# Optimization experiments

Measured on AMD Instinct MI355X. Metric: run time of the kernel, lower is better.

## Reference

```python
import jax, jax.numpy as jnp
import numpy as np

HIDDEN = 450
DEPTH = 4
ATOM_FDIM = 35
BOND_FDIM = 5
MAX_NB = 15
N_ATOMS = 30000
N_BONDS = 60000
N_MESS = 10001
N_MOLS = 1000
EPS = 1e-5


def setup_inputs() -> dict:
    key = jax.random.key(0)
    ks = jax.random.split(key, 10)
    fatoms = jax.random.normal(ks[0], (N_ATOMS, ATOM_FDIM), dtype=jnp.float32)
    fbonds = jax.random.normal(ks[1], (N_BONDS, ATOM_FDIM + BOND_FDIM), dtype=jnp.float32)
    # indices into concatenated [tree_message; graph_message] table (index 0 = zero pad slot)
    agraph = jax.random.randint(ks[2], (N_ATOMS, MAX_NB), 0, N_MESS + N_BONDS)
    bgraph = jax.random.randint(ks[3], (N_BONDS, MAX_NB), 0, N_MESS + N_BONDS)
    per_mol = N_ATOMS // N_MOLS
    starts = jnp.arange(N_MOLS, dtype=jnp.int64) * per_mol
    lens = jnp.full((N_MOLS,), per_mol, dtype=jnp.int64)
    scope = jnp.stack([starts, lens], axis=1)
    tree_message = jax.random.normal(ks[4], (N_MESS, HIDDEN), dtype=jnp.float32)
    tree_message = tree_message.at[0].set(0.0)  # padding row
    s = 0.05
    W_i = jax.random.normal(ks[5], (HIDDEN, ATOM_FDIM + BOND_FDIM), dtype=jnp.float32) * s
    W_h = jax.random.normal(ks[6], (HIDDEN, HIDDEN), dtype=jnp.float32) * s
    W_o = jax.random.normal(ks[7], (HIDDEN, ATOM_FDIM + HIDDEN), dtype=jnp.float32) * s
    b_o = jax.random.normal(ks[8], (HIDDEN,), dtype=jnp.float32) * s
    gamma = jnp.ones((HIDDEN,), dtype=jnp.float32)
    beta = jnp.zeros((HIDDEN,), dtype=jnp.float32)
    return {"fatoms": fatoms, "fbonds": fbonds, "agraph": agraph, "bgraph": bgraph,
            "scope": scope, "tree_message": tree_message, "W_i": W_i, "W_h": W_h,
            "W_o": W_o, "b_o": b_o, "gamma": gamma, "beta": beta}


def reference(fatoms, fbonds, agraph, bgraph, scope, tree_message, W_i, W_h, W_o, b_o, gamma, beta):
    # bond input features -> hidden
    binput = fbonds @ W_i.T                      # [n_bonds, H]
    graph_message = jax.nn.relu(binput)
    # message-passing loop (dropout is identity in eval / p=0)
    for _ in range(DEPTH - 1):
        message = jnp.concatenate([tree_message, graph_message], axis=0)
        nei = message[bgraph].sum(axis=1)        # padded-neighbor gather + sum -> [n_bonds, H]
        graph_message = jax.nn.relu(binput + nei @ W_h.T)
    message = jnp.concatenate([tree_message, graph_message], axis=0)
    nei = message[agraph].sum(axis=1)            # [n_atoms, H]
    ainput = jnp.concatenate([fatoms, nei], axis=1)
    h = ainput @ W_o.T + b_o                     # [n_atoms, H]
    # BatchNorm1d (training-mode batch statistics, biased variance)
    mean = h.mean(axis=0)
    var = ((h - mean) ** 2).mean(axis=0)
    h = (h - mean) * jax.lax.rsqrt(var + EPS) * gamma + beta
    h = jax.nn.relu(h)
    # scope-based segment mean pooling
    starts = scope[:, 0]
    lens = scope[:, 1]
    mol_id = jnp.searchsorted(starts, jnp.arange(N_ATOMS), side="right") - 1
    sums = jax.ops.segment_sum(h, mol_id, num_segments=N_MOLS)
    denom = jnp.maximum(lens, 1).astype(h.dtype)[:, None]
    return jnp.where(lens[:, None] > 0, sums / denom, jnp.zeros_like(sums))
```

## Files before the change

### kernel.cpp

```cpp
#include <hip/hip_runtime.h>
#include <cstdint>
#include <cstddef>

#define HIDDEN 450
#define ATOM_FDIM 35
#define IN_FDIM 40
#define MAX_NB 15
#define N_ATOMS 30000
#define N_BONDS 60000
#define N_MESS 10001
#define N_MOLS 1000
#define DEPTH 4
#define NTOT (N_MESS + N_BONDS)

#define KPAD 512
#define MLD  464
#define MB_PAD 60032
#define MA_PAD 30080

typedef _Float16 f16x8_t __attribute__((ext_vector_type(8)));
typedef float f32x4_t __attribute__((ext_vector_type(4)));
typedef unsigned short ushort8_t __attribute__((ext_vector_type(8)));

__device__ __forceinline__ float h2f(unsigned short u) {
    return (float)__builtin_bit_cast(_Float16, u);
}
__device__ __forceinline__ unsigned short f2h(float f) {
    return __builtin_bit_cast(unsigned short, (_Float16)f);
}
__device__ __forceinline__ void st_out(unsigned short* p, float v) { *p = f2h(v); }
__device__ __forceinline__ void st_out(float* p, float v) { *p = v; }

__device__ __forceinline__ void g2l16(const unsigned short* g, unsigned short* l) {
    __builtin_amdgcn_global_load_lds(
        (const __attribute__((address_space(1))) void*)g,
        (__attribute__((address_space(3))) void*)l, 16, 0, 0);
}

__device__ __forceinline__ bool sniff_is64(const void* g) {
    const int* g32 = (const int*)g;
    return (g32[1] | g32[3] | g32[5] | g32[7]) == 0;
}
__device__ __forceinline__ long long load_idx(const void* g, size_t pos, bool is64) {
    return is64 ? ((const long long*)g)[pos] : (long long)((const int*)g)[pos];
}

__global__ void zero_stats_kernel(float* __restrict__ p) {
    int i = blockIdx.x * blockDim.x + threadIdx.x;
    if (i < 2 * HIDDEN) p[i] = 0.f;
}

__global__ void build_wih_kernel(const float* __restrict__ W_i,
                                 const float* __restrict__ W_h,
                                 unsigned short* __restrict__ Wih) {
    int t = blockIdx.x * blockDim.x + threadIdx.x;
    if (t >= KPAD * KPAD) return;
    int n = t >> 9, k = t & 511;
    float v = 0.f;
    if (n < HIDDEN) {
        if (k < IN_FDIM)            v = W_i[(size_t)n * IN_FDIM + k];
        else if (k < IN_FDIM + HIDDEN) v = W_h[(size_t)n * HIDDEN + (k - IN_FDIM)];
    }
    Wih[t] = f2h(v);
}

__global__ void build_wo_kernel(const float* __restrict__ W_o,
                                unsigned short* __restrict__ Wo) {
    int t = blockIdx.x * blockDim.x + threadIdx.x;
    if (t >= KPAD * KPAD) return;
    int n = t >> 9, k = t & 511;
    float v = 0.f;
    if (n < HIDDEN) {
        if (k < ATOM_FDIM)                   v = W_o[(size_t)n * (ATOM_FDIM + HIDDEN) + k];
        else if (k >= IN_FDIM && k < IN_FDIM + HIDDEN)
            v = W_o[(size_t)n * (ATOM_FDIM + HIDDEN) + ATOM_FDIM + (k - IN_FDIM)];
    }
    Wo[t] = f2h(v);
}

__global__ void cvt_fbonds_kernel(const float* __restrict__ fbonds,
                                  unsigned short* __restrict__ Ab) {
    int t = blockIdx.x * blockDim.x + threadIdx.x;
    if (t >= MB_PAD * 64) return;
    int r = t >> 6, c8 = (t & 63) * 8;
    ushort8_t o;
    #pragma unroll
    for (int j = 0; j < 8; ++j) {
        int c = c8 + j;
        float v = (r < N_BONDS && c < IN_FDIM) ? fbonds[(size_t)r * IN_FDIM + c] : 0.f;
        o[j] = f2h(v);
    }
    *(ushort8_t*)(Ab + (size_t)r * KPAD + c8) = o;
}

__global__ void cvt_fatoms_kernel(const float* __restrict__ fatoms,
                                  unsigned short* __restrict__ Aa) {
    int t = blockIdx.x * blockDim.x + threadIdx.x;
    if (t >= MA_PAD * 64) return;
    int r = t >> 6, c8 = (t & 63) * 8;
    ushort8_t o;
    #pragma unroll
    for (int j = 0; j < 8; ++j) {
        int c = c8 + j;
        float v = (r < N_ATOMS && c < ATOM_FDIM) ? fatoms[(size_t)r * ATOM_FDIM + c] : 0.f;
        o[j] = f2h(v);
    }
    *(ushort8_t*)(Aa + (size_t)r * KPAD + c8) = o;
}

__global__ void cvt_tree_kernel(const float* __restrict__ tree,
                                unsigned short* __restrict__ tb) {
    int t = blockIdx.x * blockDim.x + threadIdx.x;
    if (t >= N_MESS * (MLD / 8)) return;
    int r = t / (MLD / 8), c8 = (t % (MLD / 8)) * 8;
    ushort8_t o;
    #pragma unroll
    for (int j = 0; j < 8; ++j) {
        int c = c8 + j;
        float v = (c < HIDDEN) ? tree[(size_t)r * HIDDEN + c] : 0.f;
        o[j] = f2h(v);
    }
    *(ushort8_t*)(tb + (size_t)r * MLD + c8) = o;
}

__global__ void zero_gmpad_kernel(unsigned short* __restrict__ gm) {
    int r = blockIdx.x * blockDim.x + threadIdx.x;
    if (r >= N_BONDS) return;
    ushort8_t z = {0, 0, 0, 0, 0, 0, 0, 0};
    *(ushort8_t*)(gm + (size_t)r * MLD + 448) = z;
    *(ushort8_t*)(gm + (size_t)r * MLD + 456) = z;
}

template<bool RELU, bool BIAS, typename OT>
__global__ __launch_bounds__(256)
void mfma_gemm_kernel(const unsigned short* __restrict__ A,
                      const unsigned short* __restrict__ B,
                      const float* __restrict__ bias,
                      OT* __restrict__ Out, int ldo,
                      int M, int Nvalid, int K)
{
    __shared__ unsigned short As[128 * 32];
    __shared__ unsigned short Bs[128 * 32];
    const int tid  = threadIdx.x;
    const int wave = tid >> 6, lane = tid & 63;
    const int m0 = blockIdx.x * 128, n0 = blockIdx.y * 128;
    const int wm = wave >> 1, wn = wave & 1;

    const unsigned short* At = A + (size_t)m0 * KPAD;
    const unsigned short* Bt = B + (size_t)n0 * KPAD;

    const int c0 = wave * 128 + lane;
    const int c1 = c0 + 64;
    const int rA0 = c0 >> 2, kc0 = (c0 & 3) * 8;
    const int rA1 = c1 >> 2, kc1 = (c1 & 3) * 8;
    unsigned short* lA0 = &As[(size_t)(wave * 128) * 8];
    unsigned short* lA1 = &As[(size_t)(wave * 128 + 64) * 8];
    unsigned short* lB0 = &Bs[(size_t)(wave * 128) * 8];
    unsigned short* lB1 = &Bs[(size_t)(wave * 128 + 64) * 8];

    const int fr = lane & 15, kof = (lane >> 4) * 8;

    f32x4_t acc[4][4];
    #pragma unroll
    for (int mi = 0; mi < 4; ++mi)
        #pragma unroll
        for (int ni = 0; ni < 4; ++ni)
            acc[mi][ni] = f32x4_t{0.f, 0.f, 0.f, 0.f};

    for (int k0 = 0; k0 < K; k0 += 32) {
        g2l16(At + (size_t)rA0 * KPAD + k0 + kc0, lA0);
        g2l16(At + (size_t)rA1 * KPAD + k0 + kc1, lA1);
        g2l16(Bt + (size_t)rA0 * KPAD + k0 + kc0, lB0);
        g2l16(Bt + (size_t)rA1 * KPAD + k0 + kc1, lB1);
        __syncthreads();

        f16x8_t a[4], b[4];
        #pragma unroll
        for (int mi = 0; mi < 4; ++mi)
            a[mi] = __builtin_bit_cast(f16x8_t,
                *(const ushort8_t*)&As[(size_t)((wm * 64 + mi * 16 + fr) * 32 + kof)]);
        #pragma unroll
        for (int ni = 0; ni < 4; ++ni)
            b[ni] = __builtin_bit_cast(f16x8_t,
                *(const ushort8_t*)&Bs[(size_t)((wn * 64 + ni * 16 + fr) * 32 + kof)]);
        #pragma unroll
        for (int mi = 0; mi < 4; ++mi)
            #pragma unroll
            for (int ni = 0; ni < 4; ++ni)
                acc[mi][ni] = __builtin_amdgcn_mfma_f32_16x16x32_f16(
                    a[mi], b[ni], acc[mi][ni], 0, 0, 0);
        __syncthreads();
    }

    #pragma unroll
    for (int mi = 0; mi < 4; ++mi) {
        int row_b = m0 + wm * 64 + mi * 16 + (lane >> 4) * 4;
        #pragma unroll
        for (int ni = 0; ni < 4; ++ni) {
            int col = n0 + wn * 64 + ni * 16 + fr;
            if (col >= Nvalid) continue;
            float bi = BIAS ? bias[col] : 0.f;
            #pragma unroll
            for (int r = 0; r < 4; ++r) {
                int row = row_b + r;
                if (row >= M) continue;
                float v = acc[mi][ni][r] + bi;
                if (RELU) v = fmaxf(v, 0.f);
                st_out(&Out[(size_t)row * ldo + col], v);
            }
        }
    }
}

__global__ __launch_bounds__(256)
void gather_kernel(const void* __restrict__ graph, int n_rows,
                   const unsigned short* __restrict__ tree,
                   const unsigned short* __restrict__ gm,
                   unsigned short* __restrict__ Adst)
{
    const bool is64 = sniff_is64(graph);
    int w    = (int)((blockIdx.x * 256 + threadIdx.x) >> 6);
    int lane = threadIdx.x & 63;
    if (w >= n_rows) return;
    const bool act = lane < 57;
    const size_t coff = (size_t)(act ? lane : 0) * 8;

    const unsigned short* rp[MAX_NB];
    #pragma unroll
    for (int nb = 0; nb < MAX_NB; ++nb) {
        long long idx = load_idx(graph, (size_t)w * MAX_NB + nb, is64);
        if (idx < 0) idx = 0;
        if (idx >= NTOT) idx = NTOT - 1;
        int i32 = __builtin_amdgcn_readfirstlane((int)idx);
        rp[nb] = (i32 < N_MESS) ? tree + (size_t)i32 * MLD
                                : gm + (size_t)(i32 - N_MESS) * MLD;
    }
    ushort8_t v[MAX_NB];
    #pragma unroll
    for (int nb = 0; nb < MAX_NB; ++nb)
        v[nb] = *(const ushort8_t*)(rp[nb] + coff);

    float acc[8] = {};
    #pragma unroll
    for (int nb = 0; nb < MAX_NB; ++nb)
        #pragma unroll
        for (int j = 0; j < 8; ++j)
            acc[j] += h2f(v[nb][j]);

    if (act) {
        ushort8_t o;
        #pragma unroll
        for (int j = 0; j < 8; ++j) o[j] = f2h(acc[j]);
        *(ushort8_t*)(Adst + (size_t)w * KPAD + IN_FDIM + (size_t)lane * 8) = o;
    }
}

__global__ __launch_bounds__(256)
void colstats_kernel(const float* __restrict__ h,
                     float* __restrict__ sums, float* __restrict__ sumsq)
{
    int t = threadIdx.x;
    int r0 = blockIdx.x * 250;
    float s0 = 0.f, q0 = 0.f, s1 = 0.f, q1 = 0.f;
    bool has1 = t < HIDDEN - 256;
    for (int r = r0; r < r0 + 250; ++r) {
        const float* row = h + (size_t)r * HIDDEN;
        float v0 = row[t];
        s0 += v0; q0 += v0 * v0;
        if (has1) {
            float v1 = row[t + 256];
            s1 += v1; q1 += v1 * v1;
        }
    }
    atomicAdd(&sums[t], s0);
    atomicAdd(&sumsq[t], q0);
    if (has1) {
        atomicAdd(&sums[t + 256], s1);
        atomicAdd(&sumsq[t + 256], q1);
    }
}

__global__ void finalize_stats_kernel(const float* __restrict__ sums,
                                      const float* __restrict__ sumsq,
                                      const float* __restrict__ gamma,
                                      const float* __restrict__ beta,
                                      float* __restrict__ scale,
                                      float* __restrict__ shift)
{
    int c = blockIdx.x * blockDim.x + threadIdx.x;
    if (c >= HIDDEN) return;
    float mean = sums[c] * (1.f / N_ATOMS);
    float var  = sumsq[c] * (1.f / N_ATOMS) - mean * mean;
    float inv  = rsqrtf(var + 1e-5f);
    float sc   = gamma[c] * inv;
    scale[c] = sc;
    shift[c] = beta[c] - mean * sc;
}

__global__ __launch_bounds__(256)
void pool_kernel(const float* __restrict__ h, const void* __restrict__ scope,
                 const float* __restrict__ scale, const float* __restrict__ shift,
                 float* __restrict__ out)
{
    int m = blockIdx.x;
    const int* s32 = (const int*)scope;
    bool is64 = (s32[1] == 0 && s32[3] == 0);
    long long start, len, nxt;
    if (is64) {
        const long long* s = (const long long*)scope;
        start = s[2 * m]; len = s[2 * m + 1];
        nxt = (m < N_MOLS - 1) ? s[2 * m + 2] : (long long)N_ATOMS;
    } else {
        start = s32[2 * m]; len = s32[2 * m + 1];
        nxt = (m < N_MOLS - 1) ? (long long)s32[2 * m + 2] : (long long)N_ATOMS;
    }
    if (start < 0) start = 0;
    if (nxt > N_ATOMS) nxt = N_ATOMS;

    int t = threadIdx.x;
    bool has1 = t < HIDDEN - 256;
    float sc0 = scale[t], sh0 = shift[t];
    float sc1 = 0.f, sh1 = 0.f;
    if (has1) { sc1 = scale[t + 256]; sh1 = shift[t + 256]; }
    float a0 = 0.f, a1 = 0.f;
    for (long long r = start; r < nxt; ++r) {
        const float* row = h + (size_t)r * HIDDEN;
        a0 += fmaxf(fmaf(row[t], sc0, sh0), 0.f);
        if (has1) a1 += fmaxf(fmaf(row[t + 256], sc1, sh1), 0.f);
    }
    float den = (float)(len > 0 ? len : 1);
    out[(size_t)m * HIDDEN + t] = (len > 0) ? a0 / den : 0.f;
    if (has1) out[(size_t)m * HIDDEN + t + 256] = (len > 0) ? a1 / den : 0.f;
}

extern "C" void kernel_launch(void* const* d_in, const int* in_sizes, int n_in,
                              void* d_out, int out_size, void* d_ws, size_t ws_size,
                              hipStream_t stream)
{
    const float* fatoms = (const float*)d_in[0];
    const float* fbonds = (const float*)d_in[1];
    const void*  agraph = d_in[2];
    const void*  bgraph = d_in[3];
    const void*  scope  = d_in[4];
    const float* tree   = (const float*)d_in[5];
    const float* W_i    = (const float*)d_in[6];
    const float* W_h    = (const float*)d_in[7];
    const float* W_o    = (const float*)d_in[8];
    const float* b_o    = (const float*)d_in[9];
    const float* gamma  = (const float*)d_in[10];
    const float* beta   = (const float*)d_in[11];
    float* out = (float*)d_out;

    char* ws = (char*)d_ws;
    size_t off = 0;
    auto alloc = [&](size_t bytes) { char* p = ws + off; off += (bytes + 255) & ~(size_t)255; return p; };
    float*          sums  = (float*)alloc(4 * HIDDEN * sizeof(float));
    float*          sumsq = sums + HIDDEN;
    float*          scale = sums + 2 * HIDDEN;
    float*          shift = sums + 3 * HIDDEN;
    unsigned short* Abond = (unsigned short*)alloc((size_t)MB_PAD * KPAD * 2);
    unsigned short* Aatom = (unsigned short*)alloc((size_t)MA_PAD * KPAD * 2);
    unsigned short* gm    = (unsigned short*)alloc((size_t)N_BONDS * MLD * 2);
    unsigned short* tb    = (unsigned short*)alloc((size_t)N_MESS * MLD * 2);
    unsigned short* Wih   = (unsigned short*)alloc((size_t)KPAD * KPAD * 2);
    unsigned short* Wo    = (unsigned short*)alloc((size_t)KPAD * KPAD * 2);
    float*          h     = (float*)alloc((size_t)N_ATOMS * HIDDEN * sizeof(float));
    (void)ws_size;

    dim3 blk(256);

    zero_stats_kernel<<<4, blk, 0, stream>>>(sums);
    build_wih_kernel<<<(KPAD * KPAD + 255) / 256, blk, 0, stream>>>(W_i, W_h, Wih);
    build_wo_kernel<<<(KPAD * KPAD + 255) / 256, blk, 0, stream>>>(W_o, Wo);
    cvt_fbonds_kernel<<<(MB_PAD * 64 + 255) / 256, blk, 0, stream>>>(fbonds, Abond);
    cvt_fatoms_kernel<<<(MA_PAD * 64 + 255) / 256, blk, 0, stream>>>(fatoms, Aatom);
    cvt_tree_kernel<<<(N_MESS * (MLD / 8) + 255) / 256, blk, 0, stream>>>(tree, tb);
    zero_gmpad_kernel<<<(N_BONDS + 255) / 256, blk, 0, stream>>>(gm);

    dim3 gBond(MB_PAD / 128, 4);
    dim3 gAtom(MA_PAD / 128, 4);

    mfma_gemm_kernel<true, false, unsigned short><<<gBond, blk, 0, stream>>>(
        Abond, Wih, nullptr, gm, MLD, N_BONDS, HIDDEN, 64);

    for (int it = 0; it < DEPTH - 1; ++it) {
        gather_kernel<<<N_BONDS / 4, blk, 0, stream>>>(bgraph, N_BONDS, tb, gm, Abond);
        mfma_gemm_kernel<true, false, unsigned short><<<gBond, blk, 0, stream>>>(
            Abond, Wih, nullptr, gm, MLD, N_BONDS, HIDDEN, KPAD);
    }

    gather_kernel<<<N_ATOMS / 4, blk, 0, stream>>>(agraph, N_ATOMS, tb, gm, Aatom);
    mfma_gemm_kernel<false, true, float><<<gAtom, blk, 0, stream>>>(
        Aatom, Wo, b_o, h, HIDDEN, N_ATOMS, HIDDEN, KPAD);

    colstats_kernel<<<120, blk, 0, stream>>>(h, sums, sumsq);
    finalize_stats_kernel<<<1, 512, 0, stream>>>(sums, sumsq, gamma, beta, scale, shift);
    pool_kernel<<<N_MOLS, blk, 0, stream>>>(h, scope, scale, shift, out);
}
```

Before: 849.4 us.

## Pad message rows to 512, swizzle GEMM tile order, store h in fp16, trim conversions

Message tables now use a 512-element row stride instead of 464, so gather rows are 1 KB aligned and all 64 lanes load. The GEMM grid becomes 1D with a grouped mapping that runs 8 M-tiles across all 4 N-tiles together, which should improve L2 reuse of the A tiles. The atom GEMM output h is now stored in fp16, halving traffic for the stats and pooling kernels at some cost in precision. The fbonds and fatoms conversions now write only the feature and tail columns instead of whole padded rows.

New measurement: 800.5 us (median of 2 runs). 1.06x faster.

```diff
diff --git a/kernel.cpp b/kernel.cpp
--- a/kernel.cpp
+++ b/kernel.cpp
@@ -14,7 +14,6 @@
 #define NTOT (N_MESS + N_BONDS)
 
 #define KPAD 512
-#define MLD  464
 #define MB_PAD 60032
 #define MA_PAD 30080
 
@@ -81,38 +80,40 @@
 __global__ void cvt_fbonds_kernel(const float* __restrict__ fbonds,
                                   unsigned short* __restrict__ Ab) {
     int t = blockIdx.x * blockDim.x + threadIdx.x;
-    if (t >= MB_PAD * 64) return;
-    int r = t >> 6, c8 = (t & 63) * 8;
+    if (t >= MB_PAD * 10) return;
+    int r = t / 10, c = t % 10;
+    int col0 = (c < 8) ? c * 8 : 496 + (c - 8) * 8;
     ushort8_t o;
     #pragma unroll
     for (int j = 0; j < 8; ++j) {
-        int c = c8 + j;
-        float v = (r < N_BONDS && c < IN_FDIM) ? fbonds[(size_t)r * IN_FDIM + c] : 0.f;
+        int cc = col0 + j;
+        float v = (r < N_BONDS && cc < IN_FDIM) ? fbonds[(size_t)r * IN_FDIM + cc] : 0.f;
         o[j] = f2h(v);
     }
-    *(ushort8_t*)(Ab + (size_t)r * KPAD + c8) = o;
+    *(ushort8_t*)(Ab + (size_t)r * KPAD + col0) = o;
 }
 
 __global__ void cvt_fatoms_kernel(const float* __restrict__ fatoms,
                                   unsigned short* __restrict__ Aa) {
     int t = blockIdx.x * blockDim.x + threadIdx.x;
-    if (t >= MA_PAD * 64) return;
-    int r = t >> 6, c8 = (t & 63) * 8;
+    if (t >= MA_PAD * 7) return;
+    int r = t / 7, c = t % 7;
+    int col0 = (c < 5) ? c * 8 : 496 + (c - 5) * 8;
     ushort8_t o;
     #pragma unroll
     for (int j = 0; j < 8; ++j) {
-        int c = c8 + j;
-        float v = (r < N_ATOMS && c < ATOM_FDIM) ? fatoms[(size_t)r * ATOM_FDIM + c] : 0.f;
+        int cc = col0 + j;
+        float v = (r < N_ATOMS && cc < ATOM_FDIM) ? fatoms[(size_t)r * ATOM_FDIM + cc] : 0.f;
         o[j] = f2h(v);
     }
-    *(ushort8_t*)(Aa + (size_t)r * KPAD + c8) = o;
+    *(ushort8_t*)(Aa + (size_t)r * KPAD + col0) = o;
 }
 
 __global__ void cvt_tree_kernel(const float* __restrict__ tree,
                                 unsigned short* __restrict__ tb) {
     int t = blockIdx.x * blockDim.x + threadIdx.x;
-    if (t >= N_MESS * (MLD / 8)) return;
-    int r = t / (MLD / 8), c8 = (t % (MLD / 8)) * 8;
+    if (t >= N_MESS * 64) return;
+    int r = t >> 6, c8 = (t & 63) * 8;
     ushort8_t o;
     #pragma unroll
     for (int j = 0; j < 8; ++j) {
@@ -120,15 +121,15 @@
         float v = (c < HIDDEN) ? tree[(size_t)r * HIDDEN + c] : 0.f;
         o[j] = f2h(v);
     }
-    *(ushort8_t*)(tb + (size_t)r * MLD + c8) = o;
+    *(ushort8_t*)(tb + (size_t)r * KPAD + c8) = o;
 }
 
 __global__ void zero_gmpad_kernel(unsigned short* __restrict__ gm) {
-    int r = blockIdx.x * blockDim.x + threadIdx.x;
-    if (r >= N_BONDS) return;
+    int t = blockIdx.x * blockDim.x + threadIdx.x;
+    if (t >= N_BONDS * 8) return;
+    int r = t >> 3, c = 448 + (t & 7) * 8;
     ushort8_t z = {0, 0, 0, 0, 0, 0, 0, 0};
-    *(ushort8_t*)(gm + (size_t)r * MLD + 448) = z;
-    *(ushort8_t*)(gm + (size_t)r * MLD + 456) = z;
+    *(ushort8_t*)(gm + (size_t)r * KPAD + c) = z;
 }
 
 template<bool RELU, bool BIAS, typename OT>
@@ -137,13 +138,18 @@
                       const unsigned short* __restrict__ B,
                       const float* __restrict__ bias,
                       OT* __restrict__ Out, int ldo,
-                      int M, int Nvalid, int K)
+                      int M, int Nvalid, int K, int mtiles)
 {
     __shared__ unsigned short As[128 * 32];
     __shared__ unsigned short Bs[128 * 32];
+    const int g = blockIdx.x;
+    const int mt = (g >> 5) * 8 + (g & 7);
+    const int nt = (g >> 3) & 3;
+    if (mt >= mtiles) return;
+    const int m0 = mt * 128, n0 = nt * 128;
+
     const int tid  = threadIdx.x;
     const int wave = tid >> 6, lane = tid & 63;
-    const int m0 = blockIdx.x * 128, n0 = blockIdx.y * 128;
     const int wm = wave >> 1, wn = wave & 1;
 
     const unsigned short* At = A + (size_t)m0 * KPAD;
@@ -222,8 +228,7 @@
     int w    = (int)((blockIdx.x * 256 + threadIdx.x) >> 6);
     int lane = threadIdx.x & 63;
     if (w >= n_rows) return;
-    const bool act = lane < 57;
-    const size_t coff = (size_t)(act ? lane : 0) * 8;
+    const size_t coff = (size_t)lane * 8;
 
     const unsigned short* rp[MAX_NB];
     #pragma unroll
@@ -232,8 +237,8 @@
         if (idx < 0) idx = 0;
         if (idx >= NTOT) idx = NTOT - 1;
         int i32 = __builtin_amdgcn_readfirstlane((int)idx);
-        rp[nb] = (i32 < N_MESS) ? tree + (size_t)i32 * MLD
-                                : gm + (size_t)(i32 - N_MESS) * MLD;
+        rp[nb] = (i32 < N_MESS) ? tree + (size_t)i32 * KPAD
+                                : gm + (size_t)(i32 - N_MESS) * KPAD;
     }
     ushort8_t v[MAX_NB];
     #pragma unroll
@@ -247,16 +252,16 @@
         for (int j = 0; j < 8; ++j)
             acc[j] += h2f(v[nb][j]);
 
-    if (act) {
+    if (lane < 57) {
         ushort8_t o;
         #pragma unroll
         for (int j = 0; j < 8; ++j) o[j] = f2h(acc[j]);
-        *(ushort8_t*)(Adst + (size_t)w * KPAD + IN_FDIM + (size_t)lane * 8) = o;
+        *(ushort8_t*)(Adst + (size_t)w * KPAD + IN_FDIM + coff) = o;
     }
 }
 
 __global__ __launch_bounds__(256)
-void colstats_kernel(const float* __restrict__ h,
+void colstats_kernel(const unsigned short* __restrict__ h,
                      float* __restrict__ sums, float* __restrict__ sumsq)
 {
     int t = threadIdx.x;
@@ -264,11 +269,11 @@
     float s0 = 0.f, q0 = 0.f, s1 = 0.f, q1 = 0.f;
     bool has1 = t < HIDDEN - 256;
     for (int r = r0; r < r0 + 250; ++r) {
-        const float* row = h + (size_t)r * HIDDEN;
-        float v0 = row[t];
+        const unsigned short* row = h + (size_t)r * HIDDEN;
+        float v0 = h2f(row[t]);
         s0 += v0; q0 += v0 * v0;
         if (has1) {
-            float v1 = row[t + 256];
+            float v1 = h2f(row[t + 256]);
             s1 += v1; q1 += v1 * v1;
         }
     }
@@ -298,7 +303,7 @@
 }
 
 __global__ __launch_bounds__(256)
-void pool_kernel(const float* __restrict__ h, const void* __restrict__ scope,
+void pool_kernel(const unsigned short* __restrict__ h, const void* __restrict__ scope,
                  const float* __restrict__ scale, const float* __restrict__ shift,
                  float* __restrict__ out)
 {
@@ -324,9 +329,9 @@
     if (has1) { sc1 = scale[t + 256]; sh1 = shift[t + 256]; }
     float a0 = 0.f, a1 = 0.f;
     for (long long r = start; r < nxt; ++r) {
-        const float* row = h + (size_t)r * HIDDEN;
-        a0 += fmaxf(fmaf(row[t], sc0, sh0), 0.f);
-        if (has1) a1 += fmaxf(fmaf(row[t + 256], sc1, sh1), 0.f);
+        const unsigned short* row = h + (size_t)r * HIDDEN;
+        a0 += fmaxf(fmaf(h2f(row[t]), sc0, sh0), 0.f);
+        if (has1) a1 += fmaxf(fmaf(h2f(row[t + 256]), sc1, sh1), 0.f);
     }
     float den = (float)(len > 0 ? len : 1);
     out[(size_t)m * HIDDEN + t] = (len > 0) ? a0 / den : 0.f;
@@ -360,11 +365,11 @@
     float*          shift = sums + 3 * HIDDEN;
     unsigned short* Abond = (unsigned short*)alloc((size_t)MB_PAD * KPAD * 2);
     unsigned short* Aatom = (unsigned short*)alloc((size_t)MA_PAD * KPAD * 2);
-    unsigned short* gm    = (unsigned short*)alloc((size_t)N_BONDS * MLD * 2);
-    unsigned short* tb    = (unsigned short*)alloc((size_t)N_MESS * MLD * 2);
+    unsigned short* gm    = (unsigned short*)alloc((size_t)N_BONDS * KPAD * 2);
+    unsigned short* tb    = (unsigned short*)alloc((size_t)N_MESS * KPAD * 2);
     unsigned short* Wih   = (unsigned short*)alloc((size_t)KPAD * KPAD * 2);
     unsigned short* Wo    = (unsigned short*)alloc((size_t)KPAD * KPAD * 2);
-    float*          h     = (float*)alloc((size_t)N_ATOMS * HIDDEN * sizeof(float));
+    unsigned short* h     = (unsigned short*)alloc((size_t)N_ATOMS * HIDDEN * 2);
     (void)ws_size;
 
     dim3 blk(256);
@@ -372,26 +377,26 @@
     zero_stats_kernel<<<4, blk, 0, stream>>>(sums);
     build_wih_kernel<<<(KPAD * KPAD + 255) / 256, blk, 0, stream>>>(W_i, W_h, Wih);
     build_wo_kernel<<<(KPAD * KPAD + 255) / 256, blk, 0, stream>>>(W_o, Wo);
-    cvt_fbonds_kernel<<<(MB_PAD * 64 + 255) / 256, blk, 0, stream>>>(fbonds, Abond);
-    cvt_fatoms_kernel<<<(MA_PAD * 64 + 255) / 256, blk, 0, stream>>>(fatoms, Aatom);
-    cvt_tree_kernel<<<(N_MESS * (MLD / 8) + 255) / 256, blk, 0, stream>>>(tree, tb);
-    zero_gmpad_kernel<<<(N_BONDS + 255) / 256, blk, 0, stream>>>(gm);
-
-    dim3 gBond(MB_PAD / 128, 4);
-    dim3 gAtom(MA_PAD / 128, 4);
+    cvt_fbonds_kernel<<<(MB_PAD * 10 + 255) / 256, blk, 0, stream>>>(fbonds, Abond);
+    cvt_fatoms_kernel<<<(MA_PAD * 7 + 255) / 256, blk, 0, stream>>>(fatoms, Aatom);
+    cvt_tree_kernel<<<(N_MESS * 64 + 255) / 256, blk, 0, stream>>>(tree, tb);
+    zero_gmpad_kernel<<<(N_BONDS * 8 + 255) / 256, blk, 0, stream>>>(gm);
+
+    dim3 gBond(59 * 32);
+    dim3 gAtom(30 * 32);
 
     mfma_gemm_kernel<true, false, unsigned short><<<gBond, blk, 0, stream>>>(
-        Abond, Wih, nullptr, gm, MLD, N_BONDS, HIDDEN, 64);
+        Abond, Wih, nullptr, gm, KPAD, N_BONDS, HIDDEN, 64, 469);
 
     for (int it = 0; it < DEPTH - 1; ++it) {
         gather_kernel<<<N_BONDS / 4, blk, 0, stream>>>(bgraph, N_BONDS, tb, gm, Abond);
         mfma_gemm_kernel<true, false, unsigned short><<<gBond, blk, 0, stream>>>(
-            Abond, Wih, nullptr, gm, MLD, N_BONDS, HIDDEN, KPAD);
+            Abond, Wih, nullptr, gm, KPAD, N_BONDS, HIDDEN, KPAD, 469);
     }
 
     gather_kernel<<<N_ATOMS / 4, blk, 0, stream>>>(agraph, N_ATOMS, tb, gm, Aatom);
-    mfma_gemm_kernel<false, true, float><<<gAtom, blk, 0, stream>>>(
-        Aatom, Wo, b_o, h, HIDDEN, N_ATOMS, HIDDEN, KPAD);
+    mfma_gemm_kernel<false, true, unsigned short><<<gAtom, blk, 0, stream>>>(
+        Aatom, Wo, b_o, h, HIDDEN, N_ATOMS, HIDDEN, KPAD, 235);
 
     colstats_kernel<<<120, blk, 0, stream>>>(h, sums, sumsq);
     finalize_stats_kernel<<<1, 512, 0, stream>>>(sums, sumsq, gamma, beta, scale, shift);
```
